# Kernel optimization log

Hardware: AMD Instinct MI355X
Metric: run time of the kernel (lower is better)

Reference implementation:

```python
import jax, jax.numpy as jnp
import numpy as np

D, H, K, L, NB = 128, 8, 16, 16, 2
N, E, MN, ME = 100_000, 800_000, 1_000, 8_000
VOCAB, BT, VP = 50_000, 256, 15
_SQD, _SQK = float(np.sqrt(D)), float(np.sqrt(K))


def _segment_softmax(score, seg, num):
    m = jax.ops.segment_max(score, seg, num_segments=num)
    e = jnp.exp(score - m[seg])
    z = jax.ops.segment_sum(e, seg, num_segments=num)
    return e / (z[seg] + 1e-9)


def _meta_learner(feat, u, W2, W1):
    # latent-attention factorization: feat [n,D] -> 2d param [n,H,K], 1d param [n,H]
    w = jax.nn.softmax((feat @ u.T) / _SQD, axis=-1)  # [n,L]
    return jnp.einsum('nl,lhk->nhk', w, W2), w @ W1


def _conv(feat, src, dst, p2n, p1n, p2e, p1e, Wq, Wk, Wv, Wo):
    # HeteroAttnConv: multi-head attention message passing modulated by
    # per-node (p2n,p1n) and per-edge (p2e,p1e) meta parameters.
    n = feat.shape[0]
    q = (feat @ Wq).reshape(n, H, K) * p2n
    kf = (feat @ Wk).reshape(n, H, K)
    v = (feat @ Wv).reshape(n, H, K)
    ke = kf[src] * p2e                                   # [e,H,K]
    score = (q[dst] * ke).sum(-1) / _SQK + p1e + p1n[dst]  # [e,H]
    attn = _segment_softmax(score, dst, n)
    agg = jax.ops.segment_sum(attn[..., None] * v[src], dst, num_segments=n).reshape(n, D)
    return jax.nn.relu(agg @ Wo), ke.reshape(-1, D)


def _forward(emb, u, W2lat, W1lat, Wq_m, Wk_m, Wv_m, Wo_m, Wq, Wk, Wv, Wo,
             node_vals, meta_node_vals, src, dst, meta_src, meta_dst,
             meta_node_id, meta_edge_id, target_idx,
             static_vals, static_src, static_dst):
    # _init_meta_param: static param-name graph, copy_u/sum then meta_learner
    fs = emb[static_vals]
    agg = jax.ops.segment_sum(fs[static_src], static_dst, num_segments=VP)
    p2s, p1s = _meta_learner(agg, u, W2lat, W1lat)
    base_tw, base_n1, base_n2 = p1s[0], p1s[3], p2s[6]   # target_weight, node 1d, node 2d
    base_e1, base_e2 = p1s[9], p2s[12]                   # edge 1d, edge 2d

    meta_feat = emb[meta_node_vals]
    feat = emb[node_vals]
    # _asign_param_to_graph(meta_graph): broadcast base buffers only
    mp2n = jnp.broadcast_to(base_n2, (MN, H, K))
    mp1n = jnp.broadcast_to(base_n1, (MN, H))
    mp2e = jnp.broadcast_to(base_e2, (ME, H, K))
    mp1e = jnp.broadcast_to(base_e1, (ME, H))

    out = jnp.zeros((BT, 1), feat.dtype)
    for b in range(NB):
        pre_meta, pre = meta_feat, feat
        meta_feat, meta_edge_feat = _conv(meta_feat, meta_src, meta_dst,
                                          mp2n, mp1n, mp2e, mp1e,
                                          Wq_m[b], Wk_m[b], Wv_m[b], Wo_m[b])
        # _asign_param_to_graph(graph, meta_node_feat, meta_edge_feat):
        # base repeat + indexed add of meta_learner outputs
        p2mn, p1mn = _meta_learner(meta_feat, u, W2lat, W1lat)
        p2me, p1me = _meta_learner(meta_edge_feat, u, W2lat, W1lat)
        p2n = base_n2[None] + p2mn[meta_node_id]
        p1n = base_n1[None] + p1mn[meta_node_id]
        tw = base_tw[None] + p1mn[meta_node_id]
        p2e = base_e2[None] + p2me[meta_edge_id]
        p1e = base_e1[None] + p1me[meta_edge_id]
        feat, _ = _conv(feat, src, dst, p2n, p1n, p2e, p1e,
                        Wq[b], Wk[b], Wv[b], Wo[b])
        # block residual
        meta_feat = meta_feat + pre_meta
        feat = feat + pre
        # Target: per-target-node weighted readout with target_weight param
        logit = jnp.einsum('th,thk->t', tw[target_idx],
                           feat[target_idx].reshape(BT, H, K))
        out = out + logit[:, None]
    return out / NB


def setup_inputs() -> dict:
    key = jax.random.key(0)
    ks = jax.random.split(key, 24)
    s = 0.05
    inp = {}
    inp['emb'] = jax.random.normal(ks[0], (VOCAB, D), jnp.float32) * s
    inp['u'] = jax.random.normal(ks[1], (L, D), jnp.float32) * s
    inp['W2lat'] = jax.random.normal(ks[2], (L, H, K), jnp.float32) * s
    inp['W1lat'] = jax.random.normal(ks[3], (L, H), jnp.float32) * s
    for i, nm in enumerate(['Wq_m', 'Wk_m', 'Wv_m', 'Wo_m', 'Wq', 'Wk', 'Wv', 'Wo']):
        inp[nm] = jax.random.normal(ks[4 + i], (NB, D, D), jnp.float32) / np.sqrt(D)
    inp['node_vals'] = jax.random.randint(ks[12], (N,), 0, VOCAB)
    inp['meta_node_vals'] = jax.random.randint(ks[13], (MN,), 0, VOCAB)
    inp['src'] = jax.random.randint(ks[14], (E,), 0, N)
    inp['dst'] = jax.random.randint(ks[15], (E,), 0, N)
    inp['meta_src'] = jax.random.randint(ks[16], (ME,), 0, MN)
    inp['meta_dst'] = jax.random.randint(ks[17], (ME,), 0, MN)
    inp['meta_node_id'] = jax.random.randint(ks[18], (N,), 0, MN)
    inp['meta_edge_id'] = jax.random.randint(ks[19], (E,), 0, ME)
    inp['target_idx'] = jax.random.randint(ks[20], (BT,), 0, N)
    # static param-name graph: 5 names x (1 name node + 2 token nodes), tokens->name
    name_pos = np.arange(5) * 3
    inp['static_vals'] = jax.random.randint(ks[21], (VP,), 0, VOCAB)
    inp['static_src'] = jnp.asarray(np.stack([name_pos + 1, name_pos + 2], 1).reshape(-1), jnp.int32)
    inp['static_dst'] = jnp.asarray(np.repeat(name_pos, 2), jnp.int32)
    return inp


def reference(emb, u, W2lat, W1lat, Wq_m, Wk_m, Wv_m, Wo_m, Wq, Wk, Wv, Wo,
              node_vals, meta_node_vals, src, dst, meta_src, meta_dst,
              meta_node_id, meta_edge_id, target_idx,
              static_vals, static_src, static_dst):
    return _forward(emb, u, W2lat, W1lat, Wq_m, Wk_m, Wv_m, Wo_m, Wq, Wk, Wv, Wo,
                    node_vals, meta_node_vals, src, dst, meta_src, meta_dst,
                    meta_node_id, meta_edge_id, target_idx,
                    static_vals, static_src, static_dst)
```

## Files before the change

### kernel.cpp

```cpp
#include <hip/hip_runtime.h>
#include <hip/hip_bf16.h>
#include <hip/hip_fp8.h>

#define DD   128
#define HH   8

typedef short bf16x8 __attribute__((ext_vector_type(8)));
typedef float f32x4  __attribute__((ext_vector_type(4)));
typedef float f32x2  __attribute__((ext_vector_type(2)));

__device__ __forceinline__ float b2f(unsigned short v){
  union { unsigned int u; float f; } x; x.u = ((unsigned int)v) << 16; return x.f;
}
__device__ __forceinline__ unsigned short f2b(float f){
  __hip_bfloat16 h = __float2bfloat16(f);
  return *(unsigned short*)&h;
}
__device__ __forceinline__ unsigned char f2f8(float x){
  __hip_fp8_e4m3 h(x);
  return h.__x;
}
__device__ __forceinline__ float f82f(unsigned char b){
  __hip_fp8_e4m3 h; h.__x = b;
  return (float)h;
}
__device__ __forceinline__ f32x2 bfpair(unsigned int g){
  union { unsigned int u; float f; } lo, hi;
  lo.u = g << 16; hi.u = g & 0xffff0000u;
  return (f32x2){lo.f, hi.f};
}
__device__ __forceinline__ void cvt8(uint2 w, f32x2* o){
#if defined(__has_builtin)
# if __has_builtin(__builtin_amdgcn_cvt_pk_f32_fp8)
  o[0] = __builtin_amdgcn_cvt_pk_f32_fp8((int)w.x, false);
  o[1] = __builtin_amdgcn_cvt_pk_f32_fp8((int)w.x, true);
  o[2] = __builtin_amdgcn_cvt_pk_f32_fp8((int)w.y, false);
  o[3] = __builtin_amdgcn_cvt_pk_f32_fp8((int)w.y, true);
  return;
# endif
#endif
  o[0] = (f32x2){f82f(w.x&0xff),        f82f((w.x>>8)&0xff)};
  o[1] = (f32x2){f82f((w.x>>16)&0xff),  f82f((w.x>>24)&0xff)};
  o[2] = (f32x2){f82f(w.y&0xff),        f82f((w.y>>8)&0xff)};
  o[3] = (f32x2){f82f((w.y>>16)&0xff),  f82f((w.y>>24)&0xff)};
}
struct __align__(8) us4 { unsigned short x,y,z,w; };

__device__ __forceinline__ float gld(const void* p, size_t i, bool f32){
  if (f32) return ((const float*)p)[i];
  return b2f(((const unsigned short*)p)[i]);
}

__device__ __forceinline__ void gll16(const void* g, void* l){
  __builtin_amdgcn_global_load_lds(
      (const __attribute__((address_space(1))) unsigned int*)g,
      (__attribute__((address_space(3))) unsigned int*)l, 16, 0, 0);
}

struct WPtrs { const void* p[8]; };
__global__ __launch_bounds__(256) void w_repack16(
    WPtrs W, unsigned short* __restrict__ stage, int NBt,
    const int* __restrict__ dflag)
{
  const bool wf32 = (*dflag) != 0;
  int idx = blockIdx.x >> 6;
  int ti = idx / NBt, bi = idx - ti*NBt;
  size_t bo = (size_t)bi*DD*DD;
  int i = (blockIdx.x & 63)*256 + threadIdx.x;
  int k = i >> 7, n = i & 127;
  float x;
  if (wf32) x = ((const float*)W.p[ti])[bo + i];
  else      x = b2f(((const unsigned short*)W.p[ti])[bo + i]);
  stage[(size_t)idx*DD*DD + n*DD + k] = f2b(x);
}

enum { EPI_STORE=0, EPI_SCALE_CONST=1, EPI_SCALE_GATHER=2, EPI_RELU=3,
       EPI_RELU_RES=4, EPI_RELU_RES2=5 };

#define CPAD 132


template<int EPI, bool INB, bool OUTB>
__global__ __launch_bounds__(256) void gemm128m(
    const void* __restrict__ Av, const unsigned short* __restrict__ Bt,
    void* __restrict__ Cv, int M,
    const unsigned short* __restrict__ Rb,
    const float* __restrict__ Rf, float* __restrict__ C2)
{
  __shared__ __align__(16) unsigned short Asb[64*128];
  __shared__ __align__(16) unsigned short Btb[16896];
  const int tid = threadIdx.x;
  const int wave = tid >> 6, lane = tid & 63;
  const int row0 = blockIdx.x * 64;

  if (INB){
    const char* Ab = (const char*)Av;
    int n4 = lane >> 4, c = lane & 15;
#pragma unroll
    for (int op=0; op<4; op++){
      int rA = wave*16 + op*4;
      int n = rA + n4;
      int gr = row0 + n; if (gr >= M) gr = M - 1;
      gll16(Ab + (size_t)gr*256 + ((size_t)((c ^ (n & 7)) << 4)), &Asb[rA*128]);
    }
  } else {
    const float* Af = (const float*)Av;
    int r = tid >> 2, cb = (tid & 3) * 32, rx = (r & 7) << 3;
    int gr = row0 + r;
#pragma unroll
    for (int j=0;j<8;j++){
      int cc = cb + j*4;
      float4 val = make_float4(0.f,0.f,0.f,0.f);
      if (gr < M) val = *(const float4*)(Af + (size_t)gr*DD + cc);
      us4 o; o.x=f2b(val.x); o.y=f2b(val.y); o.z=f2b(val.z); o.w=f2b(val.w);
      *(us4*)&Asb[r*128 + (cc ^ rx)] = o;
    }
  }
  {
    int n4 = lane >> 4, c = lane & 15;
#pragma unroll
    for (int op=0; op<8; op++){
      int rB = wave*32 + op*4;
      int n = rB + n4;
      gll16((const char*)Bt + (size_t)n*256 + ((size_t)((c ^ (n & 7)) << 4)),
            &Btb[rB*128]);
    }
  }
  __syncthreads();

  f32x4 acc[8];
#pragma unroll
  for (int t=0;t<8;t++) acc[t] = (f32x4){0.f,0.f,0.f,0.f};
  const int am = (lane & 15), kq = (lane >> 4) * 8, axr = (am & 7) << 3;
#pragma unroll
  for (int k0=0;k0<128;k0+=32){
    int xo = (k0 + kq) ^ axr;
    bf16x8 a = *(bf16x8*)&Asb[(wave*16 + am)*128 + xo];
#pragma unroll
    for (int t=0;t<8;t++){
      bf16x8 b = *(bf16x8*)&Btb[(t*16 + am)*128 + xo];
      acc[t] = __builtin_amdgcn_mfma_f32_16x16x32_bf16(a, b, acc[t], 0,0,0);
    }
  }
  __syncthreads();
  float* Cls = (float*)Btb;
  {
    int rr = wave*16 + (lane>>4)*4;
    int cc = lane & 15;
#pragma unroll
    for (int t=0;t<8;t++)
#pragma unroll
      for (int r=0;r<4;r++)
        Cls[(rr + r)*CPAD + t*16 + cc] = acc[t][r];
  }
  __syncthreads();

  {
    int r = tid >> 2, cb = (tid & 3) * 32;
    int gr = row0 + r;
    if (gr < M){
#pragma unroll
      for (int j=0;j<8;j++){
        int c = cb + j*4;
        float4 o = *(float4*)&Cls[r*CPAD + c];
        if (EPI == EPI_RELU_RES){
          us4 rb = *(const us4*)(Rb + (size_t)gr*DD + c);
          o.x=fmaxf(o.x,0.f)+b2f(rb.x); o.y=fmaxf(o.y,0.f)+b2f(rb.y);
          o.z=fmaxf(o.z,0.f)+b2f(rb.z); o.w=fmaxf(o.w,0.f)+b2f(rb.w);
        } else if (EPI == EPI_RELU_RES2){
          o.x=fmaxf(o.x,0.f); o.y=fmaxf(o.y,0.f); o.z=fmaxf(o.z,0.f); o.w=fmaxf(o.w,0.f);
          float4 rf = *(const float4*)(Rf + (size_t)gr*DD + c);
          *(float4*)(C2 + (size_t)gr*DD + c) =
              make_float4(o.x+rf.x, o.y+rf.y, o.z+rf.z, o.w+rf.w);
        }
        if (OUTB){
          us4 ob; ob.x=f2b(o.x); ob.y=f2b(o.y); ob.z=f2b(o.z); ob.w=f2b(o.w);
          *(us4*)((unsigned short*)Cv + (size_t)gr*DD + c) = ob;
        } else {
          *(float4*)((float*)Cv + (size_t)gr*DD + c) = o;
        }
      }
    }
  }
}

template<int EPIQ, bool INB, bool FP8KV>
__global__ __launch_bounds__(256) void gemm_qkv(
    const void* __restrict__ Av,
    const unsigned short* __restrict__ Btq, const unsigned short* __restrict__ Btk,
    const unsigned short* __restrict__ Btv,
    void* __restrict__ Cq, void* __restrict__ Ck, int stK,
    void* __restrict__ Cvo, int stV, int M,
    const float* __restrict__ svec, const float* __restrict__ P2,
    const int* __restrict__ gidx)
{
  __shared__ __align__(16) unsigned short Asb[64*128];
  __shared__ __align__(16) unsigned short Btb[16896];
  const int tid = threadIdx.x;
  const int wave = tid >> 6, lane = tid & 63;
  const int row0 = blockIdx.x * 64;

  if (INB){
    const char* Ab = (const char*)Av;
    int n4 = lane >> 4, c = lane & 15;
#pragma unroll
    for (int op=0; op<4; op++){
      int rA = wave*16 + op*4;
      int n = rA + n4;
      int gr = row0 + n; if (gr >= M) gr = M - 1;
      gll16(Ab + (size_t)gr*256 + ((size_t)((c ^ (n & 7)) << 4)), &Asb[rA*128]);
    }
  } else {
    const float* Af = (const float*)Av;
    int r = tid >> 2, cb = (tid & 3) * 32, rx = (r & 7) << 3;
    int gr = row0 + r;
#pragma unroll
    for (int j=0;j<8;j++){
      int cc = cb + j*4;
      float4 val = make_float4(0.f,0.f,0.f,0.f);
      if (gr < M) val = *(const float4*)(Af + (size_t)gr*DD + cc);
      us4 o; o.x=f2b(val.x); o.y=f2b(val.y); o.z=f2b(val.z); o.w=f2b(val.w);
      *(us4*)&Asb[r*128 + (cc ^ rx)] = o;
    }
  }

  const unsigned short* Bts[3] = {Btq, Btk, Btv};
  void* Cs[3] = {Cq, Ck, Cvo};
  const int sts[3] = {DD, stK, stV};
  const int am = (lane & 15), kq = (lane >> 4) * 8, axr = (am & 7) << 3;

  for (int ph=0; ph<3; ph++){
    {
      const unsigned short* Bt = Bts[ph];
      int n4 = lane >> 4, c = lane & 15;
#pragma unroll
      for (int op=0; op<8; op++){
        int rB = wave*32 + op*4;
        int n = rB + n4;
        gll16((const char*)Bt + (size_t)n*256 + ((size_t)((c ^ (n & 7)) << 4)),
              &Btb[rB*128]);
      }
    }
    __syncthreads();
    f32x4 acc[8];
#pragma unroll
    for (int t=0;t<8;t++) acc[t] = (f32x4){0.f,0.f,0.f,0.f};
#pragma unroll
    for (int k0=0;k0<128;k0+=32){
      int xo = (k0 + kq) ^ axr;
      bf16x8 a = *(bf16x8*)&Asb[(wave*16 + am)*128 + xo];
#pragma unroll
      for (int t=0;t<8;t++){
        bf16x8 b = *(bf16x8*)&Btb[(t*16 + am)*128 + xo];
        acc[t] = __builtin_amdgcn_mfma_f32_16x16x32_bf16(a, b, acc[t], 0,0,0);
      }
    }
    __syncthreads();
    float* Cls = (float*)Btb;
    {
      int rr = wave*16 + (lane>>4)*4;
      int cc = lane & 15;
#pragma unroll
      for (int t=0;t<8;t++)
#pragma unroll
        for (int r=0;r<4;r++)
          Cls[(rr + r)*CPAD + t*16 + cc] = acc[t][r];
    }
    __syncthreads();
    {
      int r = tid >> 2, cb = (tid & 3) * 32;
      int gr = row0 + r;
      if (gr < M){
#pragma unroll
        for (int j=0;j<8;j++){
          int c = cb + j*4;
          float4 o = *(float4*)&Cls[r*CPAD + c];
          if (ph == 0){
            if (EPIQ == EPI_SCALE_GATHER){
              int g = gidx[gr];
              const float* p = P2 + (size_t)g*DD + c;
              o.x*=(svec[c+0]+p[0]); o.y*=(svec[c+1]+p[1]);
              o.z*=(svec[c+2]+p[2]); o.w*=(svec[c+3]+p[3]);
            } else {
              o.x*=svec[c+0]; o.y*=svec[c+1]; o.z*=svec[c+2]; o.w*=svec[c+3];
            }
          }
          if (FP8KV && ph > 0){
            unsigned char* Cb = (unsigned char*)Cs[ph];
            uchar4 ob;
            ob.x=f2f8(o.x*8.f); ob.y=f2f8(o.y*8.f);
            ob.z=f2f8(o.z*8.f); ob.w=f2f8(o.w*8.f);
            *(uchar4*)(Cb + (size_t)gr*256 + c) = ob;
          } else {
            us4 ob; ob.x=f2b(o.x); ob.y=f2b(o.y); ob.z=f2b(o.z); ob.w=f2b(o.w);
            *(us4*)((unsigned short*)Cs[ph] + (size_t)gr*sts[ph] + c) = ob;
          }
        }
      }
    }
    __syncthreads();
  }
}

__global__ __launch_bounds__(256) void k_static(
    const void* __restrict__ emb, const int* __restrict__ svals,
    const int* __restrict__ ssrc, const int* __restrict__ sdst,
    const void* __restrict__ u, const void* __restrict__ W2,
    const void* __restrict__ W1, float* __restrict__ base, int nsrc,
    int* __restrict__ dflag)
{
  __shared__ float sagg[15][128];
  __shared__ float ssc[15][16];
  __shared__ float sww[15][16];
  __shared__ int swf;
  const int t = threadIdx.x;
  if (t < 64){
    float m = 0.f;
    for (int i=t; i<128; i+=64){
      float x = fabsf(b2f(((const unsigned short*)emb)[i]));
      if (x < 1e30f) m = fmaxf(m, x);
    }
#pragma unroll
    for (int s=1;s<64;s<<=1) m = fmaxf(m, __shfl_xor(m, s, 64));
    if (t==0){ int f = (m > 1e4f) ? 1 : 0; *dflag = f; swf = f; }
  }
  for (int i=t;i<15*128;i+=256) ((float*)sagg)[i]=0.f;
  __syncthreads();
  const bool wf32 = (swf != 0);
  if (t < 128){
    for (int i=0;i<nsrc;i++){
      int row = sdst[i]; int vr = svals[ssrc[i]];
      sagg[row][t] += gld(emb, (size_t)vr*DD + t, wf32);
    }
  }
  __syncthreads();
  if (t < 240){
    int n = t>>4, l = t&15;
    float a=0.f;
    for (int d=0;d<128;d++) a += sagg[n][d]*gld(u, l*128+d, wf32);
    ssc[n][l] = a * 0.08838834764831845f;
  }
  __syncthreads();
  if (t < 15){
    float mx=-1e30f;
    for (int l=0;l<16;l++) mx = fmaxf(mx, ssc[t][l]);
    float s=0.f;
    for (int l=0;l<16;l++){ float e=__expf(ssc[t][l]-mx); sww[t][l]=e; s+=e; }
    float inv = 1.f/s;
    for (int l=0;l<16;l++) sww[t][l]*=inv;
  }
  __syncthreads();
  if (t < 8){
    float a=0.f,b=0.f,c=0.f;
    for (int l=0;l<16;l++){
      float wv = gld(W1, l*8+t, wf32);
      a += sww[0][l]*wv; b += sww[3][l]*wv; c += sww[9][l]*wv;
    }
    base[t]=a; base[8+t]=b; base[16+t]=c;
  }
  if (t < 128){
    float a=0.f,b=0.f;
    for (int l=0;l<16;l++){
      float wv = gld(W2, l*128+t, wf32);
      a += sww[6][l]*wv; b += sww[12][l]*wv;
    }
    base[24+t]=a; base[152+t]=b;
  }
}

__global__ __launch_bounds__(256) void gather_rows2(
    const void* __restrict__ emb,
    const int* __restrict__ valsB, unsigned short* __restrict__ featB, int nB,
    const int* __restrict__ valsM, float* __restrict__ featM, int nM,
    const int* __restrict__ dflag)
{
  const bool wf32 = (*dflag) != 0;
  int i = blockIdx.x*256 + threadIdx.x;
  bool big = (i < nB*16);
  int i2 = big ? i : (i - nB*16);
  if (!big && i2 >= nM*16) return;
  int r = i2>>4, c = (i2&15)*8;
  int vr = big ? valsB[r] : valsM[r];
  float vb[8];
  if (wf32){
    float4 f0 = *(const float4*)((const float*)emb + (size_t)vr*DD + c);
    float4 f1 = *(const float4*)((const float*)emb + (size_t)vr*DD + c + 4);
    vb[0]=f0.x; vb[1]=f0.y; vb[2]=f0.z; vb[3]=f0.w;
    vb[4]=f1.x; vb[5]=f1.y; vb[6]=f1.z; vb[7]=f1.w;
  } else {
    uint4 raw = *(const uint4*)((const unsigned short*)emb + (size_t)vr*DD + c);
    const unsigned short* hw = (const unsigned short*)&raw;
#pragma unroll
    for (int j=0;j<8;j++) vb[j] = b2f(hw[j]);
  }
  if (big){
    unsigned short* d = featB + (size_t)r*DD + c;
    us4 o0, o1;
    o0.x=f2b(vb[0]); o0.y=f2b(vb[1]); o0.z=f2b(vb[2]); o0.w=f2b(vb[3]);
    o1.x=f2b(vb[4]); o1.y=f2b(vb[5]); o1.z=f2b(vb[6]); o1.w=f2b(vb[7]);
    *(us4*)d = o0; *(us4*)(d+4) = o1;
  } else {
    float* d = featM + (size_t)r*DD + c;
    *(float4*)d     = make_float4(vb[0],vb[1],vb[2],vb[3]);
    *(float4*)(d+4) = make_float4(vb[4],vb[5],vb[6],vb[7]);
  }
}

__global__ __launch_bounds__(256) void zeroi(int* __restrict__ p, int n){
  int i = blockIdx.x*256 + threadIdx.x;
  if (i < n) p[i] = 0;
}

__global__ __launch_bounds__(256) void k_hist2(
    const int* __restrict__ dstB, const int* __restrict__ dstM,
    int* __restrict__ degB, int* __restrict__ degM, int E, int ME, int nbE){
  int b = blockIdx.x, t = threadIdx.x;
  if (b < nbE){ int i = b*256+t; if (i < E) atomicAdd(&degB[dstB[i]], 1); }
  else { int i = (b-nbE)*256+t; if (i < ME) atomicAdd(&degM[dstM[i]], 1); }
}

__global__ __launch_bounds__(256) void k_scan1b(
    const int* __restrict__ degB, int* __restrict__ rpB, int* __restrict__ bsB,
    int nB, int nbB,
    const int* __restrict__ degM, int* __restrict__ rpM, int* __restrict__ bsM,
    int nM){
  __shared__ int ls[256];
  int blk = blockIdx.x, t = threadIdx.x;
  const int* deg; int* rowptr; int* bsum; int n; int b;
  if (blk < nbB){ deg=degB; rowptr=rpB; bsum=bsB; n=nB; b=blk; }
  else          { deg=degM; rowptr=rpM; bsum=bsM; n=nM; b=blk-nbB; }
  int base = b*1024 + t*4;
  int v0 = (base+0<n)?deg[base+0]:0;
  int v1 = (base+1<n)?deg[base+1]:0;
  int v2 = (base+2<n)?deg[base+2]:0;
  int v3 = (base+3<n)?deg[base+3]:0;
  int tsum = v0+v1+v2+v3;
  ls[t] = tsum; __syncthreads();
  for (int o=1;o<256;o<<=1){
    int x = (t>=o) ? ls[t-o] : 0;
    __syncthreads();
    ls[t] += x;
    __syncthreads();
  }
  int excl = ls[t]-tsum;
  if (t==255) bsum[b] = ls[255];
  if (base+0<n) rowptr[base+0]=excl;
  if (base+1<n) rowptr[base+1]=excl+v0;
  if (base+2<n) rowptr[base+2]=excl+v0+v1;
  if (base+3<n) rowptr[base+3]=excl+v0+v1+v2;
}

__global__ __launch_bounds__(256) void k_scan3b(
    int* __restrict__ rpB, const int* __restrict__ bsB, int* __restrict__ curB,
    int nB, int nb3B, int nbsB,
    int* __restrict__ rpM, const int* __restrict__ bsM, int* __restrict__ curM,
    int nM, int nbsM){
  __shared__ int spre;
  int blk = blockIdx.x, t = threadIdx.x;
  if (blk < nb3B){
    if (t == 0){
      int chunk = blk >> 2;
      int pre = 0;
      for (int j=0;j<chunk;j++) pre += bsB[j];
      spre = pre;
      if (blk == 0){
        int tot = 0;
        for (int j=0;j<nbsB;j++) tot += bsB[j];
        rpB[nB] = tot;
      }
    }
    __syncthreads();
    int i = blk*256 + t;
    if (i < nB){ int r = rpB[i] + spre; rpB[i] = r; curB[i] = r; }
  } else {
    int b2 = blk - nb3B;
    if (t == 0){
      int chunk = b2 >> 2;
      int pre = 0;
      for (int j=0;j<chunk;j++) pre += bsM[j];
      spre = pre;
      if (b2 == 0){
        int tot = 0;
        for (int j=0;j<nbsM;j++) tot += bsM[j];
        rpM[nM] = tot;
      }
    }
    __syncthreads();
    int i = b2*256 + t;
    if (i < nM){ int r = rpM[i] + spre; rpM[i] = r; curM[i] = r; }
  }
}

__global__ __launch_bounds__(256) void k_scatter2(
    const int* __restrict__ dstB, const int* __restrict__ srcB,
    const int* __restrict__ auxB, int* __restrict__ curB,
    int* __restrict__ epackB, int E, int nbE,
    const int* __restrict__ dstM, const int* __restrict__ srcM,
    int* __restrict__ curM, int* __restrict__ esrcM, int* __restrict__ eauxM,
    int ME){
  int blk = blockIdx.x, t = threadIdx.x;
  if (blk < nbE){
    int e = blk*256 + t;
    if (e < E){
      int p = atomicAdd(&curB[dstB[e]], 1);
      epackB[p] = srcB[e] | (auxB[e] << 17);
    }
  } else {
    int e = (blk-nbE)*256 + t;
    if (e < ME){
      int p = atomicAdd(&curM[dstM[e]], 1);
      esrcM[p] = srcM[e];
      eauxM[p] = e;
    }
  }
}

__global__ __launch_bounds__(256) void edge_meta_csr(
    const int* __restrict__ rowptr, const int* __restrict__ esrc,
    const int* __restrict__ eorig,
    const unsigned short* __restrict__ qm, const unsigned short* __restrict__ kfm,
    const unsigned short* __restrict__ vm,
    const float* __restrict__ base, unsigned short* __restrict__ mef,
    float* __restrict__ agg, int NM)
{
  int d = blockIdx.x*4 + (threadIdx.x>>6);
  if (d >= NM) return;
  int lane = threadIdx.x & 63;
  const float* be2 = base+152; const float* be1 = base+16; const float* bn1 = base+8;
  size_t dq = (size_t)d*DD;
  float q0 = b2f(qm[dq+lane]), q1 = b2f(qm[dq+64+lane]);
  float w0 = be2[lane], w1 = be2[64+lane];
  int h0 = lane>>4, h1 = h0+4;
  float bias0 = be1[h0] + bn1[h0];
  float bias1 = be1[h1] + bn1[h1];
  float z0=0.f, z1=0.f, a0=0.f, a1=0.f;
  int i0 = rowptr[d], i1 = rowptr[d+1];
  for (int i=i0; i<i1; i++){
    int s = esrc[i], e = eorig[i];
    size_t so=(size_t)s*DD, eo=(size_t)e*DD;
    float ke0 = b2f(kfm[so+lane])    * w0;
    float ke1 = b2f(kfm[so+64+lane]) * w1;
    mef[eo+lane]=f2b(ke0); mef[eo+64+lane]=f2b(ke1);
    float p0 = q0*ke0, p1 = q1*ke1;
#pragma unroll
    for (int m=1;m<16;m<<=1){ p0 += __shfl_xor(p0,m,64); p1 += __shfl_xor(p1,m,64); }
    float e0 = __expf(p0*0.25f + bias0);
    float e1 = __expf(p1*0.25f + bias1);
    z0 += e0; z1 += e1;
    a0 += e0*b2f(vm[so+lane]);
    a1 += e1*b2f(vm[so+64+lane]);
  }
  float inv0 = 1.f/(z0 + 1e-9f);
  float inv1 = 1.f/(z1 + 1e-9f);
  agg[dq+lane]    = a0*inv0;
  agg[dq+64+lane] = a1*inv1;
}

__global__ __launch_bounds__(128) void learner2(
    const float* __restrict__ Xa, const unsigned short* __restrict__ Xb, int Ma,
    const void* __restrict__ u, const void* __restrict__ W2,
    const void* __restrict__ W1,
    float* __restrict__ p2a, float* __restrict__ p1a,
    unsigned short* __restrict__ w2me, unsigned short* __restrict__ p1b,
    const float* __restrict__ base, const int* __restrict__ dflag)
{
  __shared__ float sX[128];
  __shared__ float st[16];
  __shared__ float sw[16];
  const bool wf32 = (*dflag) != 0;
  const int blk = blockIdx.x, t = threadIdx.x;
  const bool isB = (blk >= Ma);
  const int m = isB ? (blk - Ma) : blk;
  if (isB) sX[t] = b2f(Xb[(size_t)m*DD + t]);
  else     sX[t] = Xa[(size_t)m*DD + t];
  __syncthreads();
  int l = t>>3, j = t&7;
  float part = 0.f;
  for (int d=j*16; d<j*16+16; d++) part += sX[d]*gld(u, l*128+d, wf32);
  part += __shfl_xor(part,1,64); part += __shfl_xor(part,2,64); part += __shfl_xor(part,4,64);
  if (j==0) st[l] = part * 0.08838834764831845f;
  __syncthreads();
  float mx=-1e30f;
  for (int i=0;i<16;i++) mx = fmaxf(mx, st[i]);
  float ssum=0.f;
  for (int i=0;i<16;i++) ssum += __expf(st[i]-mx);
  float inv = 1.f/ssum;
  if (t<16) sw[t] = __expf(st[t]-mx)*inv;
  __syncthreads();
  float a=0.f;
  for (int i=0;i<16;i++) a += sw[i]*gld(W2, i*128+t, wf32);
  if (isB) w2me[(size_t)m*DD+t] = f2b(base[152+t] + a);
  else     p2a[(size_t)m*DD+t] = a;
  if (t<8){
    float bb=0.f;
    for (int i=0;i<16;i++) bb += sw[i]*gld(W1, i*8+t, wf32);
    if (isB) p1b[(size_t)m*HH+t] = f2b(bb);
    else     p1a[(size_t)m*HH+t] = bb;
  }
}

__global__ __launch_bounds__(256) void edge_fused(
    const int* __restrict__ rowptr, const int* __restrict__ epack,
    const int* __restrict__ mnid,
    const unsigned short* __restrict__ q, const unsigned char* __restrict__ kv8,
    const unsigned short* __restrict__ w2me, const unsigned short* __restrict__ p1me,
    const float* __restrict__ p1mn, const float* __restrict__ base,
    unsigned short* __restrict__ aggb, int N)
{
  int wv = blockIdx.x*4 + (threadIdx.x>>6);
  int d0 = wv*4;
  if (d0 >= N) return;
  int lane = threadIdx.x & 63;
  int grp = lane >> 4, l16 = lane & 15;
  int c8 = l16 * 8;
  int h = l16 >> 1;
  const float biash0 = base[16+h] + base[8+h];

  const int nd = (N - d0 < 4) ? (N - d0) : 4;
  int rp[5];
#pragma unroll
  for (int j=0;j<5;j++){ int ix = d0 + j; if (ix > N) ix = N; rp[j] = rowptr[ix]; }
  float bias[4];
#pragma unroll
  for (int j=0;j<4;j++){
    int ix = d0 + j; if (ix > N-1) ix = N-1;
    bias[j] = biash0 + p1mn[(size_t)mnid[ix]*HH + h];
  }

  uint4 qraw = *(const uint4*)(q + (size_t)d0*DD + c8);
  for (int dd=0; dd<nd; dd++){
    int d = d0 + dd;
    size_t dq = (size_t)d*DD;
    uint4 qcur = qraw;
    if (dd+1 < nd) qraw = *(const uint4*)(q + (size_t)(d+1)*DD + c8);
    f32x2 qv[4];
    {
      const unsigned int* qw = (const unsigned int*)&qcur;
#pragma unroll
      for (int j=0;j<4;j++) qv[j] = bfpair(qw[j]) * 0.03125f;
    }
    const float biasd = bias[dd];

    float zh = 0.f;
    f32x2 a2[4];
#pragma unroll
    for (int j=0;j<4;j++) a2[j] = (f32x2){0.f,0.f};

    int i0 = rp[dd], i1 = rp[dd+1];
    int i = i0 + grp;
    for (; i + 4 < i1; i += 8){
      unsigned int v0p = (unsigned int)epack[i];
      unsigned int v1p = (unsigned int)epack[i+4];
      int s0 = v0p & 0x1FFFF, me0 = v0p >> 17;
      int s1 = v1p & 0x1FFFF, me1 = v1p >> 17;
      size_t kvo0 = (size_t)s0*256, mo0 = (size_t)me0*DD;
      size_t kvo1 = (size_t)s1*256, mo1 = (size_t)me1*DD;
      uint2 kraw0 = *(const uint2*)(kv8 + kvo0 + c8);
      uint2 vraw0 = *(const uint2*)(kv8 + kvo0 + 128 + c8);
      uint4 wraw0 = *(const uint4*)(w2me + mo0 + c8);
      float pm0 = b2f(p1me[(size_t)me0*HH + h]);
      uint2 kraw1 = *(const uint2*)(kv8 + kvo1 + c8);
      uint2 vraw1 = *(const uint2*)(kv8 + kvo1 + 128 + c8);
      uint4 wraw1 = *(const uint4*)(w2me + mo1 + c8);
      float pm1 = b2f(p1me[(size_t)me1*HH + h]);
      f32x2 k0f[4], v0f[4], k1f[4], v1f[4];
      cvt8(kraw0, k0f); cvt8(vraw0, v0f);
      cvt8(kraw1, k1f); cvt8(vraw1, v1f);
      const unsigned int* ww0 = (const unsigned int*)&wraw0;
      const unsigned int* ww1 = (const unsigned int*)&wraw1;
      f32x2 pA2 = (f32x2){0.f,0.f}, pB2 = (f32x2){0.f,0.f};
#pragma unroll
      for (int j=0;j<4;j++){
        pA2 += qv[j] * (k0f[j] * bfpair(ww0[j]));
        pB2 += qv[j] * (k1f[j] * bfpair(ww1[j]));
      }
      float pA = pA2[0] + pA2[1];
      float pB = pB2[0] + pB2[1];
      pA += __shfl_xor(pA, 1, 64);
      pB += __shfl_xor(pB, 1, 64);
      float ex0 = __expf(pA + biasd + pm0);
      float ex1 = __expf(pB + biasd + pm1);
      zh += ex0 + ex1;
#pragma unroll
      for (int j=0;j<4;j++) a2[j] += v0f[j]*ex0 + v1f[j]*ex1;
    }
    if (i < i1){
      unsigned int vp = (unsigned int)epack[i];
      int s = vp & 0x1FFFF, me = vp >> 17;
      size_t kvo = (size_t)s*256, mo = (size_t)me*DD;
      uint2 kraw = *(const uint2*)(kv8 + kvo + c8);
      uint2 vraw = *(const uint2*)(kv8 + kvo + 128 + c8);
      uint4 wraw = *(const uint4*)(w2me + mo + c8);
      float pm = b2f(p1me[(size_t)me*HH + h]);
      f32x2 kf[4], vf[4];
      cvt8(kraw, kf); cvt8(vraw, vf);
      const unsigned int* ww = (const unsigned int*)&wraw;
      f32x2 p2 = (f32x2){0.f,0.f};
#pragma unroll
      for (int j=0;j<4;j++) p2 += qv[j] * (kf[j] * bfpair(ww[j]));
      float p = p2[0] + p2[1];
      p += __shfl_xor(p, 1, 64);
      float ex = __expf(p + biasd + pm);
      zh += ex;
#pragma unroll
      for (int j=0;j<4;j++) a2[j] += vf[j]*ex;
    }

    zh += __shfl_xor(zh, 16, 64); zh += __shfl_xor(zh, 32, 64);
    float r[8];
#pragma unroll
    for (int j=0;j<4;j++){
      float v0 = a2[j][0], v1 = a2[j][1];
      v0 += __shfl_xor(v0, 16, 64); v0 += __shfl_xor(v0, 32, 64);
      v1 += __shfl_xor(v1, 16, 64); v1 += __shfl_xor(v1, 32, 64);
      r[2*j] = v0; r[2*j+1] = v1;
    }
    if (grp == 0){
      float inv = 0.125f / (zh + 1e-9f);
      us4 o0, o1;
      o0.x=f2b(r[0]*inv); o0.y=f2b(r[1]*inv); o0.z=f2b(r[2]*inv); o0.w=f2b(r[3]*inv);
      o1.x=f2b(r[4]*inv); o1.y=f2b(r[5]*inv); o1.z=f2b(r[6]*inv); o1.w=f2b(r[7]*inv);
      *(us4*)(aggb + dq + c8)     = o0;
      *(us4*)(aggb + dq + c8 + 4) = o1;
    }
  }
}

__global__ __launch_bounds__(256) void readout(
    const int* __restrict__ tgt, const int* __restrict__ mnid,
    const unsigned short* __restrict__ featb, const float* __restrict__ p1mn,
    const float* __restrict__ base, float* __restrict__ acc,
    void* __restrict__ out, int last, float invNB, int BT,
    const int* __restrict__ dflag)
{
  int t = blockIdx.x*256 + threadIdx.x;
  int ti = t >> 4, l16 = t & 15;
  if (ti >= BT) return;
  int idx = tgt[ti]; int mn = mnid[idx];
  int h = l16 >> 1;
  float tw = base[h] + p1mn[(size_t)mn*HH + h];
  uint4 raw = *(const uint4*)(featb + (size_t)idx*DD + l16*8);
  const unsigned short* hw = (const unsigned short*)&raw;
  float s = 0.f;
#pragma unroll
  for (int j=0;j<8;j++) s += b2f(hw[j]);
  float part = tw * s;
  part += __shfl_xor(part, 1, 64);
  part += __shfl_xor(part, 2, 64);
  part += __shfl_xor(part, 4, 64);
  part += __shfl_xor(part, 8, 64);
  if (l16 == 0){
    if (!last) acc[ti] = part;
    else {
      float r = (acc[ti] + part) * invNB;
      if ((*dflag) != 0) ((float*)out)[ti] = r;
      else ((__hip_bfloat16*)out)[ti] = __float2bfloat16(r);
    }
  }
}

extern "C" void kernel_launch(void* const* d_in, const int* in_sizes, int n_in,
                              void* d_out, int out_size, void* d_ws, size_t ws_size,
                              hipStream_t stream) {
  const void* emb   = d_in[0];
  const void* u     = d_in[1];
  const void* W2lat = d_in[2];
  const void* W1lat = d_in[3];
  WPtrs wptrs;
  for (int i=0;i<8;i++) wptrs.p[i] = d_in[4+i];
  const int* node_vals      = (const int*)d_in[12];
  const int* meta_node_vals = (const int*)d_in[13];
  const int* src            = (const int*)d_in[14];
  const int* dst            = (const int*)d_in[15];
  const int* meta_src       = (const int*)d_in[16];
  const int* meta_dst       = (const int*)d_in[17];
  const int* meta_node_id   = (const int*)d_in[18];
  const int* meta_edge_id   = (const int*)d_in[19];
  const int* target_idx     = (const int*)d_in[20];
  const int* static_vals    = (const int*)d_in[21];
  const int* static_src     = (const int*)d_in[22];
  const int* static_dst     = (const int*)d_in[23];

  const int N  = in_sizes[12];
  const int MN = in_sizes[13];
  const int E  = in_sizes[14];
  const int ME = in_sizes[16];
  const int BT = in_sizes[20];
  const int NSRC = in_sizes[22];
  const int NB = in_sizes[8] / (DD*DD);

  float* ws = (float*)d_ws;
  size_t off = 0;
  auto allocf = [&](size_t n){ float* p = ws + off; off += (n + 3) & ~(size_t)3; return p; };
  auto allocb = [&](size_t n){ unsigned short* p = (unsigned short*)(ws + off); off += (((n+1)/2) + 3) & ~(size_t)3; return p; };
  auto alloci = [&](size_t n){ int* p = (int*)(ws + off); off += (n + 3) & ~(size_t)3; return p; };
  int*            dflag = (int*)ws; off += 4;
  unsigned short* feat  = allocb((size_t)N*DD);
  unsigned short* q     = allocb((size_t)N*DD);
  unsigned char*  kv8   = (unsigned char*)allocf((size_t)N*64);
  unsigned short* aggb  = allocb((size_t)N*DD);
  float*          meta_feat= allocf((size_t)MN*DD);
  float*          agg_m = allocf((size_t)MN*DD);
  unsigned short* q_m   = allocb((size_t)MN*DD);
  unsigned short* kf_m  = allocb((size_t)MN*DD);
  unsigned short* v_m   = allocb((size_t)MN*DD);
  float*          meta_out = allocf((size_t)MN*DD);
  unsigned short* mef   = allocb((size_t)ME*DD);
  float*          p2mn  = allocf((size_t)MN*DD);
  float*          p1mn  = allocf((size_t)MN*HH);
  unsigned short* w2me  = allocb((size_t)ME*DD);
  unsigned short* p1me  = allocb((size_t)ME*HH);
  float*          base  = allocf(280);
  float*          acc   = allocf((size_t)BT);
  unsigned short* wstage= allocb((size_t)8*NB*DD*DD);
  int*            rowptr= alloci((size_t)N+1);
  int*            cursor= alloci((size_t)N);
  int*            epack = alloci((size_t)E);
  int*            rowptr_m= alloci((size_t)MN+1);
  int*            cursor_m= alloci((size_t)MN);
  int*            esrc_m  = alloci((size_t)ME);
  int*            eorig_m = alloci((size_t)ME);
  int*            degAll  = alloci((size_t)(N+MN));
  int*            deg     = degAll;
  int*            deg_m   = degAll + N;
  const int nb_scan   = (N + 1023)/1024;
  const int nb_scan_m = (MN + 1023)/1024;
  int*            bsum   = alloci((size_t)nb_scan);
  int*            bsum_m = alloci((size_t)nb_scan_m);
  (void)ws_size; (void)n_in; (void)out_size;

  const float* base_n2 = base + 24;

  k_static<<<1,256,0,stream>>>(emb, static_vals, static_src, static_dst,
                               u, W2lat, W1lat, base, NSRC, dflag);
  gather_rows2<<<((N+MN)*16+255)/256,256,0,stream>>>(emb, node_vals, feat, N,
      meta_node_vals, meta_feat, MN, dflag);

  const int nbE  = (E+255)/256, nbME = (ME+255)/256;
  const int nb3B = (N+255)/256, nb3M = (MN+255)/256;
  zeroi<<<(N+MN+255)/256,256,0,stream>>>(degAll, N+MN);
  k_hist2<<<nbE+nbME,256,0,stream>>>(dst, meta_dst, deg, deg_m, E, ME, nbE);
  k_scan1b<<<nb_scan+nb_scan_m,256,0,stream>>>(deg, rowptr, bsum, N, nb_scan,
      deg_m, rowptr_m, bsum_m, MN);
  k_scan3b<<<nb3B+nb3M,256,0,stream>>>(rowptr, bsum, cursor, N, nb3B, nb_scan,
      rowptr_m, bsum_m, cursor_m, MN, nb_scan_m);
  k_scatter2<<<nbE+nbME,256,0,stream>>>(dst, src, meta_edge_id, cursor,
      epack, E, nbE, meta_dst, meta_src, cursor_m, esrc_m, eorig_m, ME);

  w_repack16<<<8*NB*64,256,0,stream>>>(wptrs, wstage, NB, dflag);

  const int gm = (MN+63)/64;
  const int gN = (N+63)/64;
  const float invNB = 1.0f/(float)NB;

  for (int b=0;b<NB;b++){
    const unsigned short* wq_m = wstage + (size_t)(0*NB+b)*DD*DD;
    const unsigned short* wk_m = wstage + (size_t)(1*NB+b)*DD*DD;
    const unsigned short* wv_m = wstage + (size_t)(2*NB+b)*DD*DD;
    const unsigned short* wo_m = wstage + (size_t)(3*NB+b)*DD*DD;
    const unsigned short* wqb  = wstage + (size_t)(4*NB+b)*DD*DD;
    const unsigned short* wkb  = wstage + (size_t)(5*NB+b)*DD*DD;
    const unsigned short* wvb  = wstage + (size_t)(6*NB+b)*DD*DD;
    const unsigned short* wob  = wstage + (size_t)(7*NB+b)*DD*DD;

    gemm_qkv<EPI_SCALE_CONST,false,false><<<gm,256,0,stream>>>(meta_feat,
        wq_m, wk_m, wv_m, q_m, kf_m, DD, v_m, DD, MN, base_n2, nullptr, nullptr);
    edge_meta_csr<<<(MN+3)/4,256,0,stream>>>(rowptr_m, esrc_m, eorig_m,
        q_m, kf_m, v_m, base, mef, agg_m, MN);
    gemm128m<EPI_RELU_RES2,false,false><<<gm,256,0,stream>>>(agg_m, wo_m,
        meta_out, MN, nullptr, meta_feat, meta_feat);
    learner2<<<MN+ME,128,0,stream>>>(meta_out, mef, MN, u, W2lat, W1lat,
        p2mn, p1mn, w2me, p1me, base, dflag);

    gemm_qkv<EPI_SCALE_GATHER,true,true><<<gN,256,0,stream>>>(feat, wqb, wkb, wvb,
        q, kv8, 0, kv8 + 128, 0, N, base_n2, p2mn, meta_node_id);
    edge_fused<<<(N+15)/16,256,0,stream>>>(rowptr, epack,
        meta_node_id, q, kv8, w2me, p1me, p1mn, base, aggb, N);
    gemm128m<EPI_RELU_RES,true,true><<<gN,256,0,stream>>>(aggb, wob, feat, N,
        feat, nullptr, nullptr);

    readout<<<(BT*16+255)/256,256,0,stream>>>(target_idx, meta_node_id, feat, p1mn,
        base, acc, d_out, (b==NB-1) ? 1 : 0, invNB, BT, dflag);
  }
}
```

Measured before the change: 673.6 us.

## Map one 16-lane group per destination node in edge aggregation

The edge_fused kernel changes its work split. Before, a wavefront walked four destination nodes one after another, spreading each node's edges across its four 16-lane groups and then combining them with cross-group shuffles. Now each 16-lane group owns one destination node and walks that node's edges alone, two at a time, which removes the cross-group reductions, the serial per-node loop and the idle lanes when degrees are low. It also drops the packed f32x2 math in favour of scalar float arrays and writes one 16-byte store per lane. The cost is that lanes in a wavefront now wait on the node with the highest degree among the four, and the packed FMA code is lost.

```diff
diff --git a/kernel.cpp b/kernel.cpp
--- a/kernel.cpp
+++ b/kernel.cpp
@@ -24,27 +24,20 @@
   __hip_fp8_e4m3 h; h.__x = b;
   return (float)h;
 }
-__device__ __forceinline__ f32x2 bfpair(unsigned int g){
-  union { unsigned int u; float f; } lo, hi;
-  lo.u = g << 16; hi.u = g & 0xffff0000u;
-  return (f32x2){lo.f, hi.f};
-}
-__device__ __forceinline__ void cvt8(uint2 w, f32x2* o){
+__device__ __forceinline__ void cvt4(unsigned int w, float* o){
 #if defined(__has_builtin)
 # if __has_builtin(__builtin_amdgcn_cvt_pk_f32_fp8)
-  o[0] = __builtin_amdgcn_cvt_pk_f32_fp8((int)w.x, false);
-  o[1] = __builtin_amdgcn_cvt_pk_f32_fp8((int)w.x, true);
-  o[2] = __builtin_amdgcn_cvt_pk_f32_fp8((int)w.y, false);
-  o[3] = __builtin_amdgcn_cvt_pk_f32_fp8((int)w.y, true);
+  f32x2 lo = __builtin_amdgcn_cvt_pk_f32_fp8((int)w, false);
+  f32x2 hi = __builtin_amdgcn_cvt_pk_f32_fp8((int)w, true);
+  o[0]=lo[0]; o[1]=lo[1]; o[2]=hi[0]; o[3]=hi[1];
   return;
 # endif
 #endif
-  o[0] = (f32x2){f82f(w.x&0xff),        f82f((w.x>>8)&0xff)};
-  o[1] = (f32x2){f82f((w.x>>16)&0xff),  f82f((w.x>>24)&0xff)};
-  o[2] = (f32x2){f82f(w.y&0xff),        f82f((w.y>>8)&0xff)};
-  o[3] = (f32x2){f82f((w.y>>16)&0xff),  f82f((w.y>>24)&0xff)};
+  o[0]=f82f(w&0xff); o[1]=f82f((w>>8)&0xff);
+  o[2]=f82f((w>>16)&0xff); o[3]=f82f((w>>24)&0xff);
 }
 struct __align__(8) us4 { unsigned short x,y,z,w; };
+struct __align__(16) us8 { unsigned short s[8]; };
 
 __device__ __forceinline__ float gld(const void* p, size_t i, bool f32){
   if (f32) return ((const float*)p)[i];
@@ -608,122 +601,93 @@
     unsigned short* __restrict__ aggb, int N)
 {
   int wv = blockIdx.x*4 + (threadIdx.x>>6);
-  int d0 = wv*4;
-  if (d0 >= N) return;
   int lane = threadIdx.x & 63;
   int grp = lane >> 4, l16 = lane & 15;
+  int d = wv*4 + grp;
+  if (d >= N) return;
   int c8 = l16 * 8;
   int h = l16 >> 1;
-  const float biash0 = base[16+h] + base[8+h];
-
-  const int nd = (N - d0 < 4) ? (N - d0) : 4;
-  int rp[5];
-#pragma unroll
-  for (int j=0;j<5;j++){ int ix = d0 + j; if (ix > N) ix = N; rp[j] = rowptr[ix]; }
-  float bias[4];
-#pragma unroll
-  for (int j=0;j<4;j++){
-    int ix = d0 + j; if (ix > N-1) ix = N-1;
-    bias[j] = biash0 + p1mn[(size_t)mnid[ix]*HH + h];
-  }
-
-  uint4 qraw = *(const uint4*)(q + (size_t)d0*DD + c8);
-  for (int dd=0; dd<nd; dd++){
-    int d = d0 + dd;
-    size_t dq = (size_t)d*DD;
-    uint4 qcur = qraw;
-    if (dd+1 < nd) qraw = *(const uint4*)(q + (size_t)(d+1)*DD + c8);
-    f32x2 qv[4];
-    {
-      const unsigned int* qw = (const unsigned int*)&qcur;
-#pragma unroll
-      for (int j=0;j<4;j++) qv[j] = bfpair(qw[j]) * 0.03125f;
-    }
-    const float biasd = bias[dd];
-
-    float zh = 0.f;
-    f32x2 a2[4];
-#pragma unroll
-    for (int j=0;j<4;j++) a2[j] = (f32x2){0.f,0.f};
-
-    int i0 = rp[dd], i1 = rp[dd+1];
-    int i = i0 + grp;
-    for (; i + 4 < i1; i += 8){
-      unsigned int v0p = (unsigned int)epack[i];
-      unsigned int v1p = (unsigned int)epack[i+4];
-      int s0 = v0p & 0x1FFFF, me0 = v0p >> 17;
-      int s1 = v1p & 0x1FFFF, me1 = v1p >> 17;
-      size_t kvo0 = (size_t)s0*256, mo0 = (size_t)me0*DD;
-      size_t kvo1 = (size_t)s1*256, mo1 = (size_t)me1*DD;
-      uint2 kraw0 = *(const uint2*)(kv8 + kvo0 + c8);
-      uint2 vraw0 = *(const uint2*)(kv8 + kvo0 + 128 + c8);
-      uint4 wraw0 = *(const uint4*)(w2me + mo0 + c8);
-      float pm0 = b2f(p1me[(size_t)me0*HH + h]);
-      uint2 kraw1 = *(const uint2*)(kv8 + kvo1 + c8);
-      uint2 vraw1 = *(const uint2*)(kv8 + kvo1 + 128 + c8);
-      uint4 wraw1 = *(const uint4*)(w2me + mo1 + c8);
-      float pm1 = b2f(p1me[(size_t)me1*HH + h]);
-      f32x2 k0f[4], v0f[4], k1f[4], v1f[4];
-      cvt8(kraw0, k0f); cvt8(vraw0, v0f);
-      cvt8(kraw1, k1f); cvt8(vraw1, v1f);
-      const unsigned int* ww0 = (const unsigned int*)&wraw0;
-      const unsigned int* ww1 = (const unsigned int*)&wraw1;
-      f32x2 pA2 = (f32x2){0.f,0.f}, pB2 = (f32x2){0.f,0.f};
-#pragma unroll
-      for (int j=0;j<4;j++){
-        pA2 += qv[j] * (k0f[j] * bfpair(ww0[j]));
-        pB2 += qv[j] * (k1f[j] * bfpair(ww1[j]));
-      }
-      float pA = pA2[0] + pA2[1];
-      float pB = pB2[0] + pB2[1];
-      pA += __shfl_xor(pA, 1, 64);
-      pB += __shfl_xor(pB, 1, 64);
-      float ex0 = __expf(pA + biasd + pm0);
-      float ex1 = __expf(pB + biasd + pm1);
-      zh += ex0 + ex1;
-#pragma unroll
-      for (int j=0;j<4;j++) a2[j] += v0f[j]*ex0 + v1f[j]*ex1;
-    }
-    if (i < i1){
-      unsigned int vp = (unsigned int)epack[i];
-      int s = vp & 0x1FFFF, me = vp >> 17;
-      size_t kvo = (size_t)s*256, mo = (size_t)me*DD;
-      uint2 kraw = *(const uint2*)(kv8 + kvo + c8);
-      uint2 vraw = *(const uint2*)(kv8 + kvo + 128 + c8);
-      uint4 wraw = *(const uint4*)(w2me + mo + c8);
-      float pm = b2f(p1me[(size_t)me*HH + h]);
-      f32x2 kf[4], vf[4];
-      cvt8(kraw, kf); cvt8(vraw, vf);
-      const unsigned int* ww = (const unsigned int*)&wraw;
-      f32x2 p2 = (f32x2){0.f,0.f};
-#pragma unroll
-      for (int j=0;j<4;j++) p2 += qv[j] * (kf[j] * bfpair(ww[j]));
-      float p = p2[0] + p2[1];
-      p += __shfl_xor(p, 1, 64);
-      float ex = __expf(p + biasd + pm);
-      zh += ex;
-#pragma unroll
-      for (int j=0;j<4;j++) a2[j] += vf[j]*ex;
-    }
-
-    zh += __shfl_xor(zh, 16, 64); zh += __shfl_xor(zh, 32, 64);
-    float r[8];
-#pragma unroll
-    for (int j=0;j<4;j++){
-      float v0 = a2[j][0], v1 = a2[j][1];
-      v0 += __shfl_xor(v0, 16, 64); v0 += __shfl_xor(v0, 32, 64);
-      v1 += __shfl_xor(v1, 16, 64); v1 += __shfl_xor(v1, 32, 64);
-      r[2*j] = v0; r[2*j+1] = v1;
-    }
-    if (grp == 0){
-      float inv = 0.125f / (zh + 1e-9f);
-      us4 o0, o1;
-      o0.x=f2b(r[0]*inv); o0.y=f2b(r[1]*inv); o0.z=f2b(r[2]*inv); o0.w=f2b(r[3]*inv);
-      o1.x=f2b(r[4]*inv); o1.y=f2b(r[5]*inv); o1.z=f2b(r[6]*inv); o1.w=f2b(r[7]*inv);
-      *(us4*)(aggb + dq + c8)     = o0;
-      *(us4*)(aggb + dq + c8 + 4) = o1;
-    }
-  }
+
+  int i0 = rowptr[d], i1 = rowptr[d+1];
+  float bias = base[16+h] + base[8+h] + p1mn[(size_t)mnid[d]*HH + h];
+  size_t dq = (size_t)d*DD;
+  float qv[8];
+  {
+    uint4 qraw = *(const uint4*)(q + dq + c8);
+    const unsigned short* qh = (const unsigned short*)&qraw;
+#pragma unroll
+    for (int j=0;j<8;j++) qv[j] = b2f(qh[j])*0.03125f;
+  }
+
+  float zh = 0.f;
+  float a[8];
+#pragma unroll
+  for (int j=0;j<8;j++) a[j] = 0.f;
+
+  int i = i0;
+  for (; i + 1 < i1; i += 2){
+    unsigned int v0p = (unsigned int)epack[i];
+    unsigned int v1p = (unsigned int)epack[i+1];
+    int s0 = v0p & 0x1FFFF, me0 = v0p >> 17;
+    int s1 = v1p & 0x1FFFF, me1 = v1p >> 17;
+    size_t kvo0 = (size_t)s0*256, mo0 = (size_t)me0*DD;
+    size_t kvo1 = (size_t)s1*256, mo1 = (size_t)me1*DD;
+    uint2 kraw0 = *(const uint2*)(kv8 + kvo0 + c8);
+    uint2 vraw0 = *(const uint2*)(kv8 + kvo0 + 128 + c8);
+    uint4 wraw0 = *(const uint4*)(w2me + mo0 + c8);
+    float pm0 = b2f(p1me[(size_t)me0*HH + h]);
+    uint2 kraw1 = *(const uint2*)(kv8 + kvo1 + c8);
+    uint2 vraw1 = *(const uint2*)(kv8 + kvo1 + 128 + c8);
+    uint4 wraw1 = *(const uint4*)(w2me + mo1 + c8);
+    float pm1 = b2f(p1me[(size_t)me1*HH + h]);
+    float k0f[8], v0f[8], k1f[8], v1f[8];
+    cvt4(kraw0.x, k0f); cvt4(kraw0.y, k0f+4);
+    cvt4(vraw0.x, v0f); cvt4(vraw0.y, v0f+4);
+    cvt4(kraw1.x, k1f); cvt4(kraw1.y, k1f+4);
+    cvt4(vraw1.x, v1f); cvt4(vraw1.y, v1f+4);
+    const unsigned short* wh0 = (const unsigned short*)&wraw0;
+    const unsigned short* wh1 = (const unsigned short*)&wraw1;
+    float pA = 0.f, pB = 0.f;
+#pragma unroll
+    for (int j=0;j<8;j++){
+      pA += qv[j]*(k0f[j]*b2f(wh0[j]));
+      pB += qv[j]*(k1f[j]*b2f(wh1[j]));
+    }
+    pA += __shfl_xor(pA, 1, 64);
+    pB += __shfl_xor(pB, 1, 64);
+    float ex0 = __expf(pA + bias + pm0);
+    float ex1 = __expf(pB + bias + pm1);
+    zh += ex0 + ex1;
+#pragma unroll
+    for (int j=0;j<8;j++) a[j] += ex0*v0f[j] + ex1*v1f[j];
+  }
+  if (i < i1){
+    unsigned int vp = (unsigned int)epack[i];
+    int s = vp & 0x1FFFF, me = vp >> 17;
+    size_t kvo = (size_t)s*256, mo = (size_t)me*DD;
+    uint2 kraw = *(const uint2*)(kv8 + kvo + c8);
+    uint2 vraw = *(const uint2*)(kv8 + kvo + 128 + c8);
+    uint4 wraw = *(const uint4*)(w2me + mo + c8);
+    float pm = b2f(p1me[(size_t)me*HH + h]);
+    float kf[8], vf[8];
+    cvt4(kraw.x, kf); cvt4(kraw.y, kf+4);
+    cvt4(vraw.x, vf); cvt4(vraw.y, vf+4);
+    const unsigned short* wh = (const unsigned short*)&wraw;
+    float p = 0.f;
+#pragma unroll
+    for (int j=0;j<8;j++) p += qv[j]*(kf[j]*b2f(wh[j]));
+    p += __shfl_xor(p, 1, 64);
+    float ex = __expf(p + bias + pm);
+    zh += ex;
+#pragma unroll
+    for (int j=0;j<8;j++) a[j] += ex*vf[j];
+  }
+
+  float inv = 0.125f / (zh + 1e-9f);
+  us8 o;
+#pragma unroll
+  for (int j=0;j<8;j++) o.s[j] = f2b(a[j]*inv);
+  *(us8*)(aggb + dq + c8) = o;
 }
 
 __global__ __launch_bounds__(256) void readout(
```

After: 647.9 us. 1.04x faster.
